# Kernel optimization log

Hardware: AMD Instinct MI355X
Metric: run time of the kernel (lower is better)

Reference implementation:

```python
import jax, jax.numpy as jnp
import numpy as np

N_EMBD = 1024
N_HEAD = 16
B, T = 8, 1024
EPS = 1e-5


def setup_inputs() -> dict:
    key = jax.random.key(0)
    ks = jax.random.split(key, 12)
    C = N_EMBD
    s_in = 1.0 / np.sqrt(C)
    s_ff = 1.0 / np.sqrt(4 * C)
    inp = {
        "x": jax.random.normal(ks[0], (B, T, C), dtype=jnp.float32),
        "mask": jnp.tril(jnp.ones((T, T), dtype=jnp.int32))[None, None, :, :],
        "ln1_w": jnp.ones((C,), jnp.float32),
        "ln1_b": jnp.zeros((C,), jnp.float32),
        "ln2_w": jnp.ones((C,), jnp.float32),
        "ln2_b": jnp.zeros((C,), jnp.float32),
        "wq": jax.random.normal(ks[1], (C, C), jnp.float32) * s_in,
        "bq": jnp.zeros((C,), jnp.float32),
        "wk": jax.random.normal(ks[2], (C, C), jnp.float32) * s_in,
        "bk": jnp.zeros((C,), jnp.float32),
        "wv": jax.random.normal(ks[3], (C, C), jnp.float32) * s_in,
        "bv": jnp.zeros((C,), jnp.float32),
        "wo": jax.random.normal(ks[4], (C, C), jnp.float32) * s_in,
        "bo": jnp.zeros((C,), jnp.float32),
        "w1": jax.random.normal(ks[5], (C, 4 * C), jnp.float32) * s_in,
        "b1": jnp.zeros((4 * C,), jnp.float32),
        "w2": jax.random.normal(ks[6], (4 * C, C), jnp.float32) * s_ff,
        "b2": jnp.zeros((C,), jnp.float32),
    }
    return inp


def _layer_norm(x, w, b):
    mu = jnp.mean(x, axis=-1, keepdims=True)
    var = jnp.mean(jnp.square(x - mu), axis=-1, keepdims=True)
    return (x - mu) * jax.lax.rsqrt(var + EPS) * w + b


def reference(x, mask, ln1_w, ln1_b, ln2_w, ln2_b,
              wq, bq, wk, bk, wv, bv, wo, bo, w1, b1, w2, b2):
    Bx, Tx, C = x.shape
    H = N_HEAD
    d = C // H
    h = _layer_norm(x, ln1_w, ln1_b)
    q = (h @ wq + bq).reshape(Bx, Tx, H, d)
    k = (h @ wk + bk).reshape(Bx, Tx, H, d)
    v = (h @ wv + bv).reshape(Bx, Tx, H, d)
    # [B,H,Tq,Tk] scores, scaled by sqrt(head_dim)
    scores = jnp.einsum('bqhd,bkhd->bhqk', q, k) / jnp.sqrt(jnp.float32(d))
    scores = jnp.where(mask == 0, -jnp.inf, scores)
    attn = jax.nn.softmax(scores, axis=-1)
    ctx = jnp.einsum('bhqk,bkhd->bqhd', attn, v).reshape(Bx, Tx, C)
    x = x + (ctx @ wo + bo)
    h2 = _layer_norm(x, ln2_w, ln2_b)
    ff = jax.nn.gelu(h2 @ w1 + b1, approximate=False) @ w2 + b2
    return x + ff
```

## Files before the change

kernel.cpp:

```cpp
#include <hip/hip_runtime.h>
#include <hip/hip_bf16.h>
#include <math.h>


#define DEVI __device__ __forceinline__

typedef __attribute__((ext_vector_type(4))) float floatx4;
typedef __attribute__((ext_vector_type(16))) float floatx16;
typedef __attribute__((ext_vector_type(8))) short shortx8;

DEVI ushort f2b(float f) {
    __hip_bfloat16 h = __float2bfloat16(f);
    return __builtin_bit_cast(ushort, h);
}

DEVI void gl_lds16(const ushort* g, ushort* l) {
    __builtin_amdgcn_global_load_lds(
        (const __attribute__((address_space(1))) void*)g,
        (__attribute__((address_space(3))) void*)l, 16, 0, 0);
}

DEVI float gelu_f(float v) {
    const float u0 = 0.7978845608f * v * (1.0f + 0.044715f * v * v);
    const float u  = fminf(fmaxf(u0, -15.0f), 15.0f);
    const float e  = exp2f(u * 2.885390082f);
    const float th = 1.0f - 2.0f / (e + 1.0f);
    return 0.5f * v * (1.0f + th);
}

__global__ void transp4_kernel(const float* __restrict__ s0, const float* __restrict__ s1,
                               const float* __restrict__ s2, const float* __restrict__ s3,
                               ushort* __restrict__ d0, ushort* __restrict__ d1,
                               ushort* __restrict__ d2, ushort* __restrict__ d3) {
    const int z = blockIdx.z;
    const float* src = (z == 0) ? s0 : (z == 1) ? s1 : (z == 2) ? s2 : s3;
    ushort*      dst = (z == 0) ? d0 : (z == 1) ? d1 : (z == 2) ? d2 : d3;
    __shared__ float tile[32][33];
    const int c0 = blockIdx.x * 32, r0 = blockIdx.y * 32;
    const int tx = threadIdx.x, ty = threadIdx.y;
#pragma unroll
    for (int i = 0; i < 32; i += 8)
        tile[ty + i][tx] = src[(size_t)(r0 + ty + i) * 1024 + c0 + tx];
    __syncthreads();
#pragma unroll
    for (int i = 0; i < 32; i += 8)
        dst[(size_t)(c0 + ty + i) * 1024 + r0 + tx] = f2b(tile[tx][ty + i]);
}

__global__ void transp_kernel(const float* __restrict__ src,
                              ushort* __restrict__ dst, int R, int C) {
    __shared__ float tile[32][33];
    const int c0 = blockIdx.x * 32, r0 = blockIdx.y * 32;
    const int tx = threadIdx.x, ty = threadIdx.y;
#pragma unroll
    for (int i = 0; i < 32; i += 8)
        tile[ty + i][tx] = src[(size_t)(r0 + ty + i) * C + c0 + tx];
    __syncthreads();
#pragma unroll
    for (int i = 0; i < 32; i += 8)
        dst[(size_t)(c0 + ty + i) * R + r0 + tx] = f2b(tile[tx][ty + i]);
}

__global__ __launch_bounds__(256)
void ln_kernel(const float* __restrict__ x, const float* __restrict__ w,
               const float* __restrict__ b, ushort* __restrict__ out) {
    __shared__ float red[8];
    const int m = blockIdx.x;
    const int tid = threadIdx.x;
    const float4 xv = *(const float4*)&x[(size_t)m * 1024 + tid * 4];
    float s  = xv.x + xv.y + xv.z + xv.w;
    float s2 = xv.x * xv.x + xv.y * xv.y + xv.z * xv.z + xv.w * xv.w;
#pragma unroll
    for (int o = 32; o >= 1; o >>= 1) {
        s  += __shfl_xor(s, o, 64);
        s2 += __shfl_xor(s2, o, 64);
    }
    const int wv_ = tid >> 6;
    if ((tid & 63) == 0) { red[wv_] = s; red[4 + wv_] = s2; }
    __syncthreads();
    s  = red[0] + red[1] + red[2] + red[3];
    s2 = red[4] + red[5] + red[6] + red[7];
    const float mu   = s * (1.0f / 1024.0f);
    const float var  = s2 * (1.0f / 1024.0f) - mu * mu;
    const float rstd = rsqrtf(var + 1e-5f);
    const float4 wv = *(const float4*)&w[tid * 4];
    const float4 bv = *(const float4*)&b[tid * 4];
    ushort o4[4];
    o4[0] = f2b((xv.x - mu) * rstd * wv.x + bv.x);
    o4[1] = f2b((xv.y - mu) * rstd * wv.y + bv.y);
    o4[2] = f2b((xv.z - mu) * rstd * wv.z + bv.z);
    o4[3] = f2b((xv.w - mu) * rstd * wv.w + bv.w);
    *(uint2*)&out[(size_t)m * 1024 + tid * 4] = *(uint2*)o4;
}


#define STAGE_A(j, h) { const int c_ = (j) & 1;                                         \
    gl_lds16(pA + (size_t)((h) * 128) * K + (j) * 64,                                   \
             lds + c_ * 16384 + (h) * 8192 + dOff);                                     \
    gl_lds16(pA + (size_t)((h) * 128 + 8) * K + (j) * 64,                               \
             lds + c_ * 16384 + (h) * 8192 + dOff + 512); }

#define STAGE_B(j, h) { const int c_ = (j) & 1;                                         \
    gl_lds16(pB + (size_t)((h) * 128) * K + (j) * 64,                                   \
             lds + 32768 + c_ * 16384 + (h) * 8192 + dOff);                             \
    gl_lds16(pB + (size_t)((h) * 128 + 8) * K + (j) * 64,                               \
             lds + 32768 + c_ * 16384 + (h) * 8192 + dOff + 512); }

#define LOAD_A(mq, c) { const ushort* ap = lds + (c) * 16384 + (mq) * 8192;             \
    _Pragma("unroll") for (int mi = 0; mi < 4; ++mi) {                                  \
        af[mi][0] = *(const shortx8*)&ap[aBase + mi * 1024];                            \
        af[mi][1] = *(const shortx8*)&ap[(aBase ^ 32) + mi * 1024]; } }

#define LOAD_B(nq, c) { const ushort* bp = lds + 32768 + (c) * 16384 + (nq) * 8192;     \
    _Pragma("unroll") for (int ni = 0; ni < 2; ++ni) {                                  \
        bf[ni][0] = *(const shortx8*)&bp[bBase + ni * 1024];                            \
        bf[ni][1] = *(const shortx8*)&bp[(bBase ^ 32) + ni * 1024]; } }

#define MFMA16(mq, nq) {                                                                \
    _Pragma("unroll") for (int mi = 0; mi < 4; ++mi)                                    \
    _Pragma("unroll") for (int ni = 0; ni < 2; ++ni)                                    \
    _Pragma("unroll") for (int ks = 0; ks < 2; ++ks)                                    \
        acc[mq][mi][nq][ni] = __builtin_amdgcn_mfma_f32_16x16x32_bf16(                  \
            af[mi][ks], bf[ni][ks], acc[mq][mi][nq][ni], 0, 0, 0); }

#define PH_SYNC() { __builtin_amdgcn_s_barrier();                                       \
    asm volatile("s_waitcnt lgkmcnt(0)" ::: "memory");                                  \
    __builtin_amdgcn_sched_barrier(0); }

template <int MODE>
__global__ __launch_bounds__(512, 2)
void gemm8(const ushort* __restrict__ A, const ushort* __restrict__ Bt,
           const float* __restrict__ biasQ, const float* __restrict__ biasK,
           const float* __restrict__ biasV,
           void* __restrict__ out, void* __restrict__ out2, void* __restrict__ out3,
           int N, int K) {
    __shared__ __align__(16) ushort lds[65536];

    const int tid  = threadIdx.x;
    const int lane = tid & 63;
    const int w    = tid >> 6;
    const int wr   = w >> 2;
    const int wc   = w & 3;

    int bx = blockIdx.x, by = blockIdx.y;
    {
        const int nwg = gridDim.x * gridDim.y;
        if ((nwg & 7) == 0) {
            const int flat = by * gridDim.x + bx;
            const int cpx  = nwg >> 3;
            const int wg   = (flat & 7) * cpx + (flat >> 3);
            bx = wg % gridDim.x;
            by = wg / gridDim.x;
        }
    }
    const int m0 = by * 256;
    const int n0 = bx * 256;
    const int NT = K >> 6;

    floatx4 acc[2][4][2][2] = {};

    const int lr3 = lane >> 3;
    const int sc  = (lane & 7) ^ lr3;
    const ushort* pA = A  + (size_t)(m0 + w * 16 + lr3) * K + sc * 8;
    const ushort* pB = Bt + (size_t)(n0 + w * 16 + lr3) * K + sc * 8;
    const int dOff = w * 1024;

    const int c0    = (lane >> 4) ^ (lane & 7);
    const int aBase = (wr * 64 + (lane & 15)) * 64 + c0 * 8;
    const int bBase = (wc * 32 + (lane & 15)) * 64 + c0 * 8;

    shortx8 af[4][2], bf[2][2];

    STAGE_A(0, 0); STAGE_B(0, 1); STAGE_A(0, 1); STAGE_B(0, 0);
    STAGE_A(1, 0); STAGE_B(1, 1);

#pragma unroll 1
    for (int j = 0; j < NT; ++j) {
        const int c = j & 1;
        if (j == NT - 1) { asm volatile("s_waitcnt vmcnt(0)" ::: "memory"); }
        else             { asm volatile("s_waitcnt vmcnt(4)" ::: "memory"); }
        __builtin_amdgcn_s_barrier();

        LOAD_A(0, c); LOAD_B(0, c);
        if (j + 1 < NT) STAGE_A(j + 1, 1);
        PH_SYNC();
        __builtin_amdgcn_s_setprio(1); MFMA16(0, 0); __builtin_amdgcn_s_setprio(0);
        __builtin_amdgcn_s_barrier();

        LOAD_B(1, c);
        if (j + 1 < NT) STAGE_B(j + 1, 0);
        PH_SYNC();
        __builtin_amdgcn_s_setprio(1); MFMA16(0, 1); __builtin_amdgcn_s_setprio(0);
        __builtin_amdgcn_s_barrier();

        LOAD_A(1, c);
        if (j + 2 < NT) STAGE_A(j + 2, 0);
        PH_SYNC();
        __builtin_amdgcn_s_setprio(1); MFMA16(1, 1); __builtin_amdgcn_s_setprio(0);
        __builtin_amdgcn_s_barrier();

        LOAD_B(0, c);
        if (j + 2 < NT) STAGE_B(j + 2, 1);
        PH_SYNC();
        __builtin_amdgcn_s_setprio(1); MFMA16(1, 0); __builtin_amdgcn_s_setprio(0);
    }

    if constexpr (MODE == 3) {
        float bvals[2][2];
#pragma unroll
        for (int nq = 0; nq < 2; ++nq)
#pragma unroll
            for (int ni = 0; ni < 2; ++ni)
                bvals[nq][ni] = biasQ[n0 + nq * 128 + wc * 32 + ni * 16 + (lane & 15)];
        ushort* o = (ushort*)out;
#pragma unroll
        for (int mq = 0; mq < 2; ++mq)
#pragma unroll
        for (int mi = 0; mi < 4; ++mi)
#pragma unroll
        for (int nq = 0; nq < 2; ++nq)
#pragma unroll
        for (int ni = 0; ni < 2; ++ni) {
            const int gm0 = m0 + mq * 128 + wr * 64 + mi * 16 + (lane >> 4) * 4;
            const int gn  = n0 + nq * 128 + wc * 32 + ni * 16 + (lane & 15);
#pragma unroll
            for (int r = 0; r < 4; ++r)
                o[(size_t)(gm0 + r) * N + gn] =
                    f2b(gelu_f(acc[mq][mi][nq][ni][r] + bvals[nq][ni]));
        }
    }

    if constexpr (MODE == 1) {
        const int mat   = n0 >> 10;
        const int bb    = m0 >> 10;
        const int tbase = m0 & 1023;
        if (mat < 2) {
            const float* bp = (mat == 0) ? biasQ : biasK;
            ushort* dst = (mat == 0) ? (ushort*)out : (ushort*)out2;
            float bvals[2][2];
#pragma unroll
            for (int nq = 0; nq < 2; ++nq)
#pragma unroll
                for (int ni = 0; ni < 2; ++ni)
                    bvals[nq][ni] =
                        bp[(n0 & 1023) + nq * 128 + wc * 32 + ni * 16 + (lane & 15)];
#pragma unroll
            for (int mq = 0; mq < 2; ++mq)
#pragma unroll
            for (int mi = 0; mi < 4; ++mi)
#pragma unroll
            for (int nq = 0; nq < 2; ++nq)
#pragma unroll
            for (int ni = 0; ni < 2; ++ni) {
                const int cn = (n0 & 1023) + nq * 128 + wc * 32 + ni * 16 + (lane & 15);
                const int h = cn >> 6, dd = cn & 63;
                const int t0 = tbase + mq * 128 + wr * 64 + mi * 16 + (lane >> 4) * 4;
#pragma unroll
                for (int r = 0; r < 4; ++r)
                    dst[((size_t)(bb * 16 + h) * 1024 + t0 + r) * 64 + dd] =
                        f2b(acc[mq][mi][nq][ni][r] + bvals[nq][ni]);
            }
        } else {
            const int vb = n0 - 2048;
            ushort* T = lds;
            ushort* Vt = (ushort*)out3;
            const int dimL = wc * 32 + (lane & 15);
#pragma unroll 1
            for (int dh = 0; dh < 2; ++dh) {
                __syncthreads();
#pragma unroll
                for (int ni = 0; ni < 2; ++ni) {
                    const float bv = biasV[vb + dh * 128 + dimL + ni * 16];
#pragma unroll
                    for (int mq = 0; mq < 2; ++mq)
#pragma unroll
                    for (int mi = 0; mi < 4; ++mi) {
                        const int t0 = mq * 128 + wr * 64 + mi * 16 + (lane >> 4) * 4;
#pragma unroll
                        for (int r = 0; r < 4; ++r)
                            T[(dimL + ni * 16) * 264 + t0 + r] =
                                f2b(acc[mq][mi][dh][ni][r] + bv);
                    }
                }
                __syncthreads();
#pragma unroll
                for (int it = 0; it < 8; ++it) {
                    const int idx = it * 512 + tid;
                    const int row = idx >> 5, ch = idx & 31;
                    const uint4 vv = *(const uint4*)&T[row * 264 + ch * 8];
                    const int d  = vb + dh * 128 + row;
                    const int hh = d >> 6, dl = d & 63;
                    *(uint4*)&Vt[((size_t)(bb * 16 + hh) * 64 + dl) * 1024 + tbase + ch * 8] = vv;
                }
            }
        }
    }
}

__global__ __launch_bounds__(256)
void gemm_res(const ushort* __restrict__ A, const ushort* __restrict__ Bt,
              const float* __restrict__ bias, float* __restrict__ out,
              const float* __restrict__ resid, int N, int K) {
    __shared__ ushort lds[128 * 64 * 2];
    ushort* sA = lds;
    ushort* sB = lds + 128 * 64;

    const int tid  = threadIdx.x;
    const int lane = tid & 63;
    const int wave = tid >> 6;
    const int l31  = lane & 31;
    const int half = lane >> 5;
    const int wm   = (wave & 1) * 64;
    const int wn   = (wave >> 1) * 64;
    const int m0   = blockIdx.y * 128;
    const int n0   = blockIdx.x * 128;

    floatx16 acc[2][2] = {};

    const int lrow = lane >> 3;
    const int scb  = (lane & 7) ^ lrow;
    const ushort* Ag = A  + (size_t)(m0 + wave * 8 + lrow) * K + scb * 8;
    const ushort* Bg = Bt + (size_t)(n0 + wave * 8 + lrow) * K + scb * 8;

    for (int k0 = 0; k0 < K; k0 += 64) {
        __syncthreads();
#pragma unroll
        for (int p = 0; p < 4; ++p) {
            gl_lds16(Ag + (size_t)(p * 32) * K + k0, sA + (p * 32 + wave * 8) * 64);
            gl_lds16(Bg + (size_t)(p * 32) * K + k0, sB + (p * 32 + wave * 8) * 64);
        }
        __syncthreads();
#pragma unroll
        for (int ks = 0; ks < 4; ++ks) {
            const int cx = ks * 2 + half;
            shortx8 af[2], bf[2];
#pragma unroll
            for (int i = 0; i < 2; ++i) {
                const int r = wm + i * 32 + l31;
                af[i] = *(const shortx8*)&sA[r * 64 + (cx ^ (r & 7)) * 8];
            }
#pragma unroll
            for (int j = 0; j < 2; ++j) {
                const int r = wn + j * 32 + l31;
                bf[j] = *(const shortx8*)&sB[r * 64 + (cx ^ (r & 7)) * 8];
            }
#pragma unroll
            for (int i = 0; i < 2; ++i)
#pragma unroll
                for (int j = 0; j < 2; ++j)
                    acc[i][j] = __builtin_amdgcn_mfma_f32_32x32x16_bf16(
                        af[i], bf[j], acc[i][j], 0, 0, 0);
        }
    }
#pragma unroll
    for (int i = 0; i < 2; ++i)
#pragma unroll
        for (int j = 0; j < 2; ++j) {
            const int gn = n0 + wn + j * 32 + l31;
            const float bv = bias[gn];
#pragma unroll
            for (int reg = 0; reg < 16; ++reg) {
                const int gm = m0 + wm + i * 32 + (reg & 3) + 8 * (reg >> 2) + 4 * half;
                out[(size_t)gm * N + gn] =
                    acc[i][j][reg] + bv + resid[(size_t)gm * N + gn];
            }
        }
}

__global__ __launch_bounds__(256)
void attn_kernel(const ushort* __restrict__ Q, const ushort* __restrict__ Kk,
                 const ushort* __restrict__ Vt, ushort* __restrict__ ctx) {
    __shared__ ushort sK[64 * 64];
    __shared__ ushort sV[64 * 64];
    __shared__ ushort sP[4][16 * 72];

    const int tid  = threadIdx.x;
    const int lane = tid & 63;
    const int wave = tid >> 6;
    const int quad = lane >> 4;
    const int l15  = lane & 15;

    const int qb = 15 - (blockIdx.x >> 7);
    const int bh = blockIdx.x & 127;
    const size_t base = (size_t)bh << 16;
    const int bb = bh >> 4, h = bh & 15;

    const int lrow = lane >> 3;
    const int scb  = (lane & 7) ^ lrow;
    const ushort* Kg = Kk + base + (size_t)(wave * 8 + lrow) * 64 + scb * 8;
    const ushort* Vg = Vt + base + (size_t)(wave * 8 + lrow) * 1024 + scb * 8;

    const int qrow = qb * 64 + wave * 16 + l15;
    const shortx8 qf0 = *(const shortx8*)&Q[base + (size_t)qrow * 64 + quad * 8];
    const shortx8 qf1 = *(const shortx8*)&Q[base + (size_t)qrow * 64 + 32 + quad * 8];

    const float SC = 0.125f * 1.44269504f;

    float mstate[4], lstate[4];
    floatx4 oacc[4] = {};
#pragma unroll
    for (int r = 0; r < 4; ++r) { mstate[r] = -__builtin_inff(); lstate[r] = 0.0f; }

    for (int kt = 0; kt <= qb; ++kt) {
        __syncthreads();
#pragma unroll
        for (int p = 0; p < 2; ++p) {
            gl_lds16(Kg + (size_t)kt * 4096 + (size_t)p * 2048,
                     sK + (p * 32 + wave * 8) * 64);
            gl_lds16(Vg + (size_t)kt * 64 + (size_t)p * 32 * 1024,
                     sV + (p * 32 + wave * 8) * 64);
        }
        __syncthreads();

        floatx4 s[4];
#pragma unroll
        for (int nt = 0; nt < 4; ++nt) {
            const int r = nt * 16 + l15;
            const int c0 = quad ^ (r & 7);
            const int c1 = (4 + quad) ^ (r & 7);
            const shortx8 kf0 = *(const shortx8*)&sK[r * 64 + c0 * 8];
            const shortx8 kf1 = *(const shortx8*)&sK[r * 64 + c1 * 8];
            floatx4 z = {};
            z = __builtin_amdgcn_mfma_f32_16x16x32_bf16(qf0, kf0, z, 0, 0, 0);
            z = __builtin_amdgcn_mfma_f32_16x16x32_bf16(qf1, kf1, z, 0, 0, 0);
            s[nt] = z;
        }
#pragma unroll
        for (int nt = 0; nt < 4; ++nt)
#pragma unroll
            for (int r = 0; r < 4; ++r) {
                float sv = s[nt][r] * SC;
                if (kt == qb) {
                    const int col = nt * 16 + l15;
                    const int row = wave * 16 + quad * 4 + r;
                    if (col > row) sv = -__builtin_inff();
                }
                s[nt][r] = sv;
            }
        float mnew[4], alpha[4];
#pragma unroll
        for (int r = 0; r < 4; ++r) {
            float mt = fmaxf(fmaxf(s[0][r], s[1][r]), fmaxf(s[2][r], s[3][r]));
#pragma unroll
            for (int o = 8; o >= 1; o >>= 1) mt = fmaxf(mt, __shfl_xor(mt, o, 64));
            mnew[r]  = fmaxf(mstate[r], mt);
            alpha[r] = exp2f(mstate[r] - mnew[r]);
            mstate[r] = mnew[r];
        }
#pragma unroll
        for (int r = 0; r < 4; ++r) {
            float rs = 0.0f;
#pragma unroll
            for (int nt = 0; nt < 4; ++nt) {
                const float p = exp2f(s[nt][r] - mnew[r]);
                s[nt][r] = p;
                rs += p;
            }
#pragma unroll
            for (int o = 8; o >= 1; o >>= 1) rs += __shfl_xor(rs, o, 64);
            lstate[r] = alpha[r] * lstate[r] + rs;
#pragma unroll
            for (int dt = 0; dt < 4; ++dt) oacc[dt][r] *= alpha[r];
        }
#pragma unroll
        for (int nt = 0; nt < 4; ++nt)
#pragma unroll
            for (int r = 0; r < 4; ++r)
                sP[wave][(quad * 4 + r) * 72 + nt * 16 + l15] = f2b(s[nt][r]);
        __asm__ volatile("s_waitcnt lgkmcnt(0)" ::: "memory");
        const shortx8 pf0 = *(const shortx8*)&sP[wave][l15 * 72 + quad * 8];
        const shortx8 pf1 = *(const shortx8*)&sP[wave][l15 * 72 + 32 + quad * 8];
#pragma unroll
        for (int dt = 0; dt < 4; ++dt) {
            const int r = dt * 16 + l15;
            const int c0 = quad ^ (r & 7);
            const int c1 = (4 + quad) ^ (r & 7);
            const shortx8 v0 = *(const shortx8*)&sV[r * 64 + c0 * 8];
            const shortx8 v1 = *(const shortx8*)&sV[r * 64 + c1 * 8];
            oacc[dt] = __builtin_amdgcn_mfma_f32_16x16x32_bf16(pf0, v0, oacc[dt], 0, 0, 0);
            oacc[dt] = __builtin_amdgcn_mfma_f32_16x16x32_bf16(pf1, v1, oacc[dt], 0, 0, 0);
        }
    }
#pragma unroll
    for (int dt = 0; dt < 4; ++dt)
#pragma unroll
        for (int r = 0; r < 4; ++r) {
            const int t = qb * 64 + wave * 16 + quad * 4 + r;
            const int dim = dt * 16 + l15;
            const float v = oacc[dt][r] / lstate[r];
            ctx[(size_t)(bb * 1024 + t) * 1024 + h * 64 + dim] = f2b(v);
        }
}

extern "C" void kernel_launch(void* const* d_in, const int* in_sizes, int n_in,
                              void* d_out, int out_size, void* d_ws, size_t ws_size,
                              hipStream_t stream) {
    const float* x    = (const float*)d_in[0];
    const float* ln1w = (const float*)d_in[2];
    const float* ln1b = (const float*)d_in[3];
    const float* ln2w = (const float*)d_in[4];
    const float* ln2b = (const float*)d_in[5];
    const float* wq   = (const float*)d_in[6];
    const float* bq   = (const float*)d_in[7];
    const float* wk   = (const float*)d_in[8];
    const float* bk   = (const float*)d_in[9];
    const float* wv   = (const float*)d_in[10];
    const float* bv   = (const float*)d_in[11];
    const float* wo   = (const float*)d_in[12];
    const float* bo   = (const float*)d_in[13];
    const float* w1   = (const float*)d_in[14];
    const float* b1   = (const float*)d_in[15];
    const float* w2   = (const float*)d_in[16];
    const float* b2   = (const float*)d_in[17];

    char* ws = (char*)d_ws;
    const size_t MB = 1024 * 1024;
    ushort* WQKVT = (ushort*)(ws + 0 * MB);
    ushort* WOT   = (ushort*)(ws + 6 * MB);
    ushort* W1T   = (ushort*)(ws + 8 * MB);
    ushort* W2T   = (ushort*)(ws + 16 * MB);
    ushort* H1    = (ushort*)(ws + 24 * MB);
    ushort* H2    = H1;
    ushort* Qb    = (ushort*)(ws + 40 * MB);
    ushort* Kb    = (ushort*)(ws + 56 * MB);
    ushort* Vbt   = (ushort*)(ws + 72 * MB);
    ushort* FF1   = (ushort*)(ws + 40 * MB);
    ushort* CTX   = (ushort*)(ws + 104 * MB);

    float* xout = (float*)d_out;

    const dim3 tb(32, 8);
    transp4_kernel<<<dim3(32, 32, 4), tb, 0, stream>>>(
        wq, wk, wv, wo,
        WQKVT, WQKVT + 1024 * 1024, WQKVT + 2048 * 1024, WOT);
    transp_kernel<<<dim3(128, 32), tb, 0, stream>>>(w1, W1T, 1024, 4096);
    transp_kernel<<<dim3(32, 128), tb, 0, stream>>>(w2, W2T, 4096, 1024);

    ln_kernel<<<8192, 256, 0, stream>>>(x, ln1w, ln1b, H1);

    gemm8<1><<<dim3(12, 32), 512, 0, stream>>>(H1, WQKVT, bq, bk, bv,
                                               Qb, Kb, Vbt, 3072, 1024);

    attn_kernel<<<2048, 256, 0, stream>>>(Qb, Kb, Vbt, CTX);

    gemm_res<<<dim3(8, 64), 256, 0, stream>>>(CTX, WOT, bo, xout, x, 1024, 1024);

    ln_kernel<<<8192, 256, 0, stream>>>(xout, ln2w, ln2b, H2);

    gemm8<3><<<dim3(16, 32), 512, 0, stream>>>(H2, W1T, b1, nullptr, nullptr,
                                               FF1, nullptr, nullptr, 4096, 1024);

    gemm_res<<<dim3(8, 64), 256, 0, stream>>>(FF1, W2T, b2, xout, xout, 1024, 4096);

    (void)in_sizes; (void)n_in; (void)out_size; (void)ws_size;
}
```

Measured before the change: 572.4 us.

## Replace residual GEMM with pipelined 256x128 kernel and coalesce epilogues via LDS

Replaces the simple double-sync gemm_res with gemm8r, a 512-thread 256x128-tile kernel that uses the same software-pipelined global-to-LDS staging, XCD-aware block remapping and 16x16 MFMAs as gemm8. Its epilogue stages fp32 results in LDS so the residual read and output write happen as coalesced float4 accesses. The gemm8 MODE 1 (Q/K) and MODE 3 (GELU) epilogues also go through an LDS transpose to emit 16-byte stores instead of scattered 2-byte stores. The cost is extra barriers and LDS traffic in the epilogues, and for the N=1024 outputs a grid of only 256 blocks.

```diff
diff --git a/kernel.cpp b/kernel.cpp
--- a/kernel.cpp
+++ b/kernel.cpp
@@ -205,28 +205,42 @@
         __builtin_amdgcn_s_setprio(1); MFMA16(1, 0); __builtin_amdgcn_s_setprio(0);
     }
 
+    const int colL  = wc * 32 + (lane & 15);
+    const int rbase = wr * 64 + ((lane >> 4) << 2);
+
     if constexpr (MODE == 3) {
         float bvals[2][2];
 #pragma unroll
         for (int nq = 0; nq < 2; ++nq)
 #pragma unroll
             for (int ni = 0; ni < 2; ++ni)
-                bvals[nq][ni] = biasQ[n0 + nq * 128 + wc * 32 + ni * 16 + (lane & 15)];
+                bvals[nq][ni] = biasQ[n0 + nq * 128 + colL + ni * 16];
         ushort* o = (ushort*)out;
-#pragma unroll
-        for (int mq = 0; mq < 2; ++mq)
-#pragma unroll
-        for (int mi = 0; mi < 4; ++mi)
-#pragma unroll
-        for (int nq = 0; nq < 2; ++nq)
-#pragma unroll
-        for (int ni = 0; ni < 2; ++ni) {
-            const int gm0 = m0 + mq * 128 + wr * 64 + mi * 16 + (lane >> 4) * 4;
-            const int gn  = n0 + nq * 128 + wc * 32 + ni * 16 + (lane & 15);
-#pragma unroll
-            for (int r = 0; r < 4; ++r)
-                o[(size_t)(gm0 + r) * N + gn] =
-                    f2b(gelu_f(acc[mq][mi][nq][ni][r] + bvals[nq][ni]));
+        ushort* T = lds;
+#pragma unroll
+        for (int mq = 0; mq < 2; ++mq) {
+            __syncthreads();
+#pragma unroll
+            for (int mi = 0; mi < 4; ++mi)
+#pragma unroll
+            for (int nq = 0; nq < 2; ++nq)
+#pragma unroll
+            for (int ni = 0; ni < 2; ++ni) {
+                const int cc = nq * 128 + colL + ni * 16;
+                const int t0 = rbase + mi * 16;
+#pragma unroll
+                for (int r = 0; r < 4; ++r)
+                    T[(t0 + r) * 264 + cc] =
+                        f2b(gelu_f(acc[mq][mi][nq][ni][r] + bvals[nq][ni]));
+            }
+            __syncthreads();
+#pragma unroll
+            for (int it = 0; it < 8; ++it) {
+                const int idx = it * 512 + tid;
+                const int row = idx >> 5, ch = idx & 31;
+                const uint4 vv = *(const uint4*)&T[row * 264 + ch * 8];
+                *(uint4*)&o[(size_t)(m0 + mq * 128 + row) * N + n0 + ch * 8] = vv;
+            }
         }
     }
 
@@ -242,30 +256,42 @@
             for (int nq = 0; nq < 2; ++nq)
 #pragma unroll
                 for (int ni = 0; ni < 2; ++ni)
-                    bvals[nq][ni] =
-                        bp[(n0 & 1023) + nq * 128 + wc * 32 + ni * 16 + (lane & 15)];
-#pragma unroll
-            for (int mq = 0; mq < 2; ++mq)
-#pragma unroll
-            for (int mi = 0; mi < 4; ++mi)
-#pragma unroll
-            for (int nq = 0; nq < 2; ++nq)
-#pragma unroll
-            for (int ni = 0; ni < 2; ++ni) {
-                const int cn = (n0 & 1023) + nq * 128 + wc * 32 + ni * 16 + (lane & 15);
-                const int h = cn >> 6, dd = cn & 63;
-                const int t0 = tbase + mq * 128 + wr * 64 + mi * 16 + (lane >> 4) * 4;
-#pragma unroll
-                for (int r = 0; r < 4; ++r)
-                    dst[((size_t)(bb * 16 + h) * 1024 + t0 + r) * 64 + dd] =
-                        f2b(acc[mq][mi][nq][ni][r] + bvals[nq][ni]);
+                    bvals[nq][ni] = bp[(n0 & 1023) + nq * 128 + colL + ni * 16];
+            ushort* T = lds;
+#pragma unroll
+            for (int mq = 0; mq < 2; ++mq) {
+                __syncthreads();
+#pragma unroll
+                for (int mi = 0; mi < 4; ++mi)
+#pragma unroll
+                for (int nq = 0; nq < 2; ++nq)
+#pragma unroll
+                for (int ni = 0; ni < 2; ++ni) {
+                    const int cc = nq * 128 + colL + ni * 16;
+                    const int t0 = rbase + mi * 16;
+#pragma unroll
+                    for (int r = 0; r < 4; ++r)
+                        T[(t0 + r) * 264 + cc] =
+                            f2b(acc[mq][mi][nq][ni][r] + bvals[nq][ni]);
+                }
+                __syncthreads();
+#pragma unroll
+                for (int it = 0; it < 8; ++it) {
+                    const int idx = it * 512 + tid;
+                    const int row = idx >> 5, ch = idx & 31;
+                    const uint4 vv = *(const uint4*)&T[row * 264 + ch * 8];
+                    const int cg = (n0 & 1023) + ch * 8;
+                    const int h = cg >> 6, dd = cg & 63;
+                    const int t = tbase + mq * 128 + row;
+                    *(uint4*)&dst[((size_t)(bb * 16 + h) * 1024 + t) * 64 + dd] = vv;
+                }
             }
         } else {
             const int vb = n0 - 2048;
             ushort* T = lds;
             ushort* Vt = (ushort*)out3;
             const int dimL = wc * 32 + (lane & 15);
-#pragma unroll 1
+#pragma unroll
             for (int dh = 0; dh < 2; ++dh) {
                 __syncthreads();
 #pragma unroll
@@ -297,74 +323,116 @@
     }
 }
 
-__global__ __launch_bounds__(256)
-void gemm_res(const ushort* __restrict__ A, const ushort* __restrict__ Bt,
-              const float* __restrict__ bias, float* __restrict__ out,
-              const float* __restrict__ resid, int N, int K) {
-    __shared__ ushort lds[128 * 64 * 2];
-    ushort* sA = lds;
-    ushort* sB = lds + 128 * 64;
+
+#define STAGE_BR(j) { const int c_ = (j) & 1;                                           \
+    gl_lds16(pB + (size_t)0 * K + (j) * 64, lds + 32768 + c_ * 8192 + dOff);            \
+    gl_lds16(pB + (size_t)8 * K + (j) * 64, lds + 32768 + c_ * 8192 + dOff + 512); }
+
+#define LOAD_BR(c) { const ushort* bp = lds + 32768 + (c) * 8192;                       \
+    _Pragma("unroll") for (int ni = 0; ni < 2; ++ni) {                                  \
+        bf[ni][0] = *(const shortx8*)&bp[bBase + ni * 1024];                            \
+        bf[ni][1] = *(const shortx8*)&bp[(bBase ^ 32) + ni * 1024]; } }
+
+#define MFMA16R(mq) {                                                                   \
+    _Pragma("unroll") for (int mi = 0; mi < 4; ++mi)                                    \
+    _Pragma("unroll") for (int ni = 0; ni < 2; ++ni)                                    \
+    _Pragma("unroll") for (int ks = 0; ks < 2; ++ks)                                    \
+        acc[mq][mi][ni] = __builtin_amdgcn_mfma_f32_16x16x32_bf16(                      \
+            af[mi][ks], bf[ni][ks], acc[mq][mi][ni], 0, 0, 0); }
+
+__global__ __launch_bounds__(512, 2)
+void gemm8r(const ushort* __restrict__ A, const ushort* __restrict__ Bt,
+            const float* __restrict__ bias, float* __restrict__ out,
+            const float* __restrict__ resid, int N, int K) {
+    __shared__ __align__(16) ushort lds[49152];
 
     const int tid  = threadIdx.x;
     const int lane = tid & 63;
-    const int wave = tid >> 6;
-    const int l31  = lane & 31;
-    const int half = lane >> 5;
-    const int wm   = (wave & 1) * 64;
-    const int wn   = (wave >> 1) * 64;
-    const int m0   = blockIdx.y * 128;
-    const int n0   = blockIdx.x * 128;
-
-    floatx16 acc[2][2] = {};
-
-    const int lrow = lane >> 3;
-    const int scb  = (lane & 7) ^ lrow;
-    const ushort* Ag = A  + (size_t)(m0 + wave * 8 + lrow) * K + scb * 8;
-    const ushort* Bg = Bt + (size_t)(n0 + wave * 8 + lrow) * K + scb * 8;
-
-    for (int k0 = 0; k0 < K; k0 += 64) {
+    const int w    = tid >> 6;
+    const int wr   = w >> 2;
+    const int wc   = w & 3;
+
+    int bx = blockIdx.x, by = blockIdx.y;
+    {
+        const int nwg = gridDim.x * gridDim.y;
+        if ((nwg & 7) == 0) {
+            const int flat = by * gridDim.x + bx;
+            const int cpx  = nwg >> 3;
+            const int wg   = (flat & 7) * cpx + (flat >> 3);
+            bx = wg % gridDim.x;
+            by = wg / gridDim.x;
+        }
+    }
+    const int m0 = by * 256;
+    const int n0 = bx * 128;
+    const int NT = K >> 6;
+
+    floatx4 acc[2][4][2] = {};
+
+    const int lr3 = lane >> 3;
+    const int sc  = (lane & 7) ^ lr3;
+    const ushort* pA = A  + (size_t)(m0 + w * 16 + lr3) * K + sc * 8;
+    const ushort* pB = Bt + (size_t)(n0 + w * 16 + lr3) * K + sc * 8;
+    const int dOff = w * 1024;
+
+    const int c0    = (lane >> 4) ^ (lane & 7);
+    const int aBase = (wr * 64 + (lane & 15)) * 64 + c0 * 8;
+    const int bBase = (wc * 32 + (lane & 15)) * 64 + c0 * 8;
+
+    shortx8 af[4][2], bf[2][2];
+
+    STAGE_A(0, 0); STAGE_A(0, 1); STAGE_BR(0); STAGE_A(1, 0);
+
+#pragma unroll 1
+    for (int j = 0; j < NT; ++j) {
+        const int c = j & 1;
+        if (j == NT - 1) { asm volatile("s_waitcnt vmcnt(0)" ::: "memory"); }
+        else             { asm volatile("s_waitcnt vmcnt(2)" ::: "memory"); }
+        __builtin_amdgcn_s_barrier();
+
+        LOAD_A(0, c); LOAD_BR(c);
+        if (j + 1 < NT) { STAGE_A(j + 1, 1); STAGE_BR(j + 1); }
+        PH_SYNC();
+        __builtin_amdgcn_s_setprio(1); MFMA16R(0); __builtin_amdgcn_s_setprio(0);
+        __builtin_amdgcn_s_barrier();
+
+        LOAD_A(1, c);
+        if (j + 2 < NT) STAGE_A(j + 2, 0);
+        PH_SYNC();
+        __builtin_amdgcn_s_setprio(1); MFMA16R(1); __builtin_amdgcn_s_setprio(0);
+    }
+
+    float bvals[2];
+#pragma unroll
+    for (int ni = 0; ni < 2; ++ni)
+        bvals[ni] = bias[n0 + wc * 32 + ni * 16 + (lane & 15)];
+    float* T = (float*)lds;
+    const int colL  = wc * 32 + (lane & 15);
+    const int rbase = wr * 64 + ((lane >> 4) << 2);
+#pragma unroll
+    for (int mq = 0; mq < 2; ++mq) {
         __syncthreads();
 #pragma unroll
-        for (int p = 0; p < 4; ++p) {
-            gl_lds16(Ag + (size_t)(p * 32) * K + k0, sA + (p * 32 + wave * 8) * 64);
-            gl_lds16(Bg + (size_t)(p * 32) * K + k0, sB + (p * 32 + wave * 8) * 64);
+        for (int mi = 0; mi < 4; ++mi)
+#pragma unroll
+        for (int ni = 0; ni < 2; ++ni) {
+            const int t0 = rbase + mi * 16;
+#pragma unroll
+            for (int r = 0; r < 4; ++r)
+                T[(t0 + r) * 132 + colL + ni * 16] = acc[mq][mi][ni][r] + bvals[ni];
         }
         __syncthreads();
 #pragma unroll
-        for (int ks = 0; ks < 4; ++ks) {
-            const int cx = ks * 2 + half;
-            shortx8 af[2], bf[2];
-#pragma unroll
-            for (int i = 0; i < 2; ++i) {
-                const int r = wm + i * 32 + l31;
-                af[i] = *(const shortx8*)&sA[r * 64 + (cx ^ (r & 7)) * 8];
-            }
-#pragma unroll
-            for (int j = 0; j < 2; ++j) {
-                const int r = wn + j * 32 + l31;
-                bf[j] = *(const shortx8*)&sB[r * 64 + (cx ^ (r & 7)) * 8];
-            }
-#pragma unroll
-            for (int i = 0; i < 2; ++i)
-#pragma unroll
-                for (int j = 0; j < 2; ++j)
-                    acc[i][j] = __builtin_amdgcn_mfma_f32_32x32x16_bf16(
-                        af[i], bf[j], acc[i][j], 0, 0, 0);
-        }
-    }
-#pragma unroll
-    for (int i = 0; i < 2; ++i)
-#pragma unroll
-        for (int j = 0; j < 2; ++j) {
-            const int gn = n0 + wn + j * 32 + l31;
-            const float bv = bias[gn];
-#pragma unroll
-            for (int reg = 0; reg < 16; ++reg) {
-                const int gm = m0 + wm + i * 32 + (reg & 3) + 8 * (reg >> 2) + 4 * half;
-                out[(size_t)gm * N + gn] =
-                    acc[i][j][reg] + bv + resid[(size_t)gm * N + gn];
-            }
-        }
+        for (int it = 0; it < 8; ++it) {
+            const int idx = it * 512 + tid;
+            const int row = idx >> 5, ch = idx & 31;
+            float4 tv = *(const float4*)&T[row * 132 + ch * 4];
+            const size_t go = (size_t)(m0 + mq * 128 + row) * N + n0 + ch * 4;
+            const float4 rv = *(const float4*)&resid[go];
+            tv.x += rv.x; tv.y += rv.y; tv.z += rv.z; tv.w += rv.w;
+            *(float4*)&out[go] = tv;
+        }
+    }
 }
 
 __global__ __launch_bounds__(256)
@@ -543,14 +611,14 @@
 
     attn_kernel<<<2048, 256, 0, stream>>>(Qb, Kb, Vbt, CTX);
 
-    gemm_res<<<dim3(8, 64), 256, 0, stream>>>(CTX, WOT, bo, xout, x, 1024, 1024);
+    gemm8r<<<dim3(8, 32), 512, 0, stream>>>(CTX, WOT, bo, xout, x, 1024, 1024);
 
     ln_kernel<<<8192, 256, 0, stream>>>(xout, ln2w, ln2b, H2);
 
     gemm8<3><<<dim3(16, 32), 512, 0, stream>>>(H2, W1T, b1, nullptr, nullptr,
                                                FF1, nullptr, nullptr, 4096, 1024);
 
-    gemm_res<<<dim3(8, 64), 256, 0, stream>>>(FF1, W2T, b2, xout, xout, 1024, 4096);
+    gemm8r<<<dim3(8, 32), 512, 0, stream>>>(FF1, W2T, b2, xout, xout, 1024, 4096);
 
     (void)in_sizes; (void)n_in; (void)out_size; (void)ws_size;
 }
```

Result: faster. 483.2 us (-15.6%).
